# Kernel optimization log

Hardware: AMD Instinct MI355X
Metric: run time of the kernel (lower is better)

Reference implementation:

```python
import jax, jax.numpy as jnp
import numpy as np

NEG_SLOPE = 0.2


def gat_layer(x, src, dst, W, a_src, a_dst, b, n_nodes):
    # x: [N, F_in]; W: [F_in, H*C]; a_src/a_dst: [H, C]; b: [H*C]
    H, C = a_src.shape
    h = (x @ W).reshape(n_nodes, H, C)                    # [N, H, C]
    al_s = jnp.sum(h * a_src, axis=-1)                    # [N, H]
    al_d = jnp.sum(h * a_dst, axis=-1)                    # [N, H]
    e = jax.nn.leaky_relu(al_s[src] + al_d[dst], NEG_SLOPE)  # [E, H]
    # segment softmax over incoming edges of each dst node
    m = jax.ops.segment_max(e, dst, num_segments=n_nodes)   # [N, H]
    e = jnp.exp(e - m[dst])
    s = jax.ops.segment_sum(e, dst, num_segments=n_nodes)   # [N, H]
    alpha = e / (s[dst] + 1e-16)                             # [E, H]
    msg = h[src] * alpha[:, :, None]                         # [E, H, C]
    out = jax.ops.segment_sum(msg, dst, num_segments=n_nodes)
    return out.reshape(n_nodes, H * C) + b


def setup_inputs() -> dict:
    key = jax.random.key(0)
    ks = jax.random.split(key, 16)
    N, E = 50000, 800000
    F_in, Hd, heads, n_cls = 256, 256, 8, 64
    C = Hd // heads
    x = jax.random.normal(ks[0], (N, F_in), dtype=jnp.float32)
    edge_index = jax.random.randint(ks[1], (2, E), 0, N, dtype=jnp.int64)

    def lin(k, fin, fout):
        return jax.random.normal(k, (fin, fout), dtype=jnp.float32) / np.sqrt(fin).astype(np.float32)

    inp = {"x": x, "edge_index": edge_index}
    # layer 1: 256 -> 8 heads x 32
    inp["W1"] = lin(ks[2], F_in, Hd)
    inp["as1"] = jax.random.normal(ks[3], (heads, C), dtype=jnp.float32) * 0.1
    inp["ad1"] = jax.random.normal(ks[4], (heads, C), dtype=jnp.float32) * 0.1
    inp["b1"] = jnp.zeros((Hd,), dtype=jnp.float32)
    # layer 2: 256 -> 8 heads x 32
    inp["W2"] = lin(ks[5], Hd, Hd)
    inp["as2"] = jax.random.normal(ks[6], (heads, C), dtype=jnp.float32) * 0.1
    inp["ad2"] = jax.random.normal(ks[7], (heads, C), dtype=jnp.float32) * 0.1
    inp["b2"] = jnp.zeros((Hd,), dtype=jnp.float32)
    # layer 3: 256 -> 1 head x 64 (num_classes)
    inp["W3"] = lin(ks[8], Hd, n_cls)
    inp["as3"] = jax.random.normal(ks[9], (1, n_cls), dtype=jnp.float32) * 0.1
    inp["ad3"] = jax.random.normal(ks[10], (1, n_cls), dtype=jnp.float32) * 0.1
    inp["b3"] = jnp.zeros((n_cls,), dtype=jnp.float32)
    return inp


def reference(x, edge_index, W1, as1, ad1, b1, W2, as2, ad2, b2, W3, as3, ad3, b3):
    N = x.shape[0]
    # PyG GATConv default add_self_loops=True
    loop = jnp.arange(N, dtype=edge_index.dtype)
    src = jnp.concatenate([edge_index[0], loop])
    dst = jnp.concatenate([edge_index[1], loop])
    h = gat_layer(x, src, dst, W1, as1, ad1, b1, N)
    h = jax.nn.relu(h)  # dropout is identity at inference
    h = gat_layer(h, src, dst, W2, as2, ad2, b2, N)
    h = jax.nn.relu(h)
    out = gat_layer(h, src, dst, W3, as3, ad3, b3, N)
    return out
```

## Files before the change

### kernel.cpp

```cpp
#include <hip/hip_runtime.h>
#include <math.h>

#define NSLOPE 0.2f

typedef __attribute__((ext_vector_type(8))) short bf16x8;
typedef __attribute__((ext_vector_type(8))) unsigned short ushort8;
typedef __attribute__((ext_vector_type(4))) float f32x4;

static __device__ __forceinline__ float leaky(float e) {
    return e > 0.f ? e : NSLOPE * e;
}

static __device__ __forceinline__ float bfu(unsigned short u) {
    return __uint_as_float(((unsigned)u) << 16);
}

static __device__ __forceinline__ unsigned short f2bf_rne(float f) {
    unsigned b = __float_as_uint(f);
    unsigned r = b + 0x7fffu + ((b >> 16) & 1u);
    return (unsigned short)(r >> 16);
}

static __device__ __forceinline__ void split1(float f, unsigned short& hi,
                                              unsigned short& lo) {
    unsigned b = __float_as_uint(f);
    unsigned hb = b & 0xffff0000u;
    hi = (unsigned short)(hb >> 16);
    lo = (unsigned short)(__float_as_uint(f - __uint_as_float(hb)) >> 16);
}


__global__ void k_count(const int* __restrict__ dst, int* __restrict__ cnt, int E) {
    int i = blockIdx.x * blockDim.x + threadIdx.x;
    if (i < E) atomicAdd(&cnt[dst[i]], 1);
}

__global__ void k_scan_local(const int* __restrict__ cnt, int* __restrict__ ptr,
                             int* __restrict__ bsum, int N) {
    __shared__ int sd[256];
    int t = threadIdx.x;
    int i0 = blockIdx.x * 1024 + t * 4;
    int v0 = (i0 + 0 < N) ? cnt[i0 + 0] : 0;
    int v1 = (i0 + 1 < N) ? cnt[i0 + 1] : 0;
    int v2 = (i0 + 2 < N) ? cnt[i0 + 2] : 0;
    int v3 = (i0 + 3 < N) ? cnt[i0 + 3] : 0;
    int ts = v0 + v1 + v2 + v3;
    sd[t] = ts;
    __syncthreads();
    for (int o = 1; o < 256; o <<= 1) {
        int add = (t >= o) ? sd[t - o] : 0;
        __syncthreads();
        sd[t] += add;
        __syncthreads();
    }
    int run = sd[t] - ts;
    if (i0 + 0 < N) ptr[i0 + 0] = run; run += v0;
    if (i0 + 1 < N) ptr[i0 + 1] = run; run += v1;
    if (i0 + 2 < N) ptr[i0 + 2] = run; run += v2;
    if (i0 + 3 < N) ptr[i0 + 3] = run;
    if (t == 255) bsum[blockIdx.x] = sd[255];
}

__global__ void k_scan_add2(int* __restrict__ ptr, const int* __restrict__ bsum,
                            int N, int Et) {
    __shared__ int base;
    const int chunk = blockIdx.x >> 2;
    if (threadIdx.x == 0) {
        int s = 0;
        for (int b = 0; b < chunk; ++b) s += bsum[b];
        base = s;
    }
    __syncthreads();
    int i = blockIdx.x * 256 + threadIdx.x;
    if (i < N) ptr[i] += base;
    else if (i == N) ptr[N] = Et;
}

__global__ void k_copy(int* __restrict__ d, const int* __restrict__ s, int N) {
    int i = blockIdx.x * blockDim.x + threadIdx.x;
    if (i < N) d[i] = s[i];
}

__global__ void k_fillcsr(const int* __restrict__ ei, int* __restrict__ fptr,
                          int* __restrict__ srcs, int E, int Et) {
    int i = blockIdx.x * blockDim.x + threadIdx.x;
    if (i >= Et) return;
    int s, d;
    if (i < E) { s = ei[i]; d = ei[E + i]; }
    else       { s = d = i - E; }
    int pos = atomicAdd(&fptr[d], 1);
    srcs[pos] = s;
}

__global__ __launch_bounds__(256) void k_prep(
    int* __restrict__ cnt, int N,
    const float* __restrict__ x, unsigned short* __restrict__ xhi,
    unsigned short* __restrict__ xlo, int n8,
    const float* __restrict__ W1, unsigned short* __restrict__ w1h, unsigned short* __restrict__ w1l,
    const float* __restrict__ W2, unsigned short* __restrict__ w2h, unsigned short* __restrict__ w2l,
    const float* __restrict__ W3, unsigned short* __restrict__ w3h, unsigned short* __restrict__ w3l,
    int nset, int nsplit) {
    __shared__ float tile[32][33];
    const int b = blockIdx.x;
    const int tid = threadIdx.x;
    if (b < nset) {
        int i = b * 256 + tid;
        if (i < N) cnt[i] = 1;
    } else if (b < nset + nsplit) {
        int i = (b - nset) * 256 + tid;
        if (i < n8) {
            const float4 v0 = *reinterpret_cast<const float4*>(&x[(size_t)i * 8]);
            const float4 v1 = *reinterpret_cast<const float4*>(&x[(size_t)i * 8 + 4]);
            const float f[8] = {v0.x, v0.y, v0.z, v0.w, v1.x, v1.y, v1.z, v1.w};
            ushort8 h, l;
#pragma unroll
            for (int j = 0; j < 8; ++j) {
                unsigned short hj, lj;
                split1(f[j], hj, lj);
                h[j] = hj; l[j] = lj;
            }
            *reinterpret_cast<ushort8*>(&xhi[(size_t)i * 8]) = h;
            *reinterpret_cast<ushort8*>(&xlo[(size_t)i * 8]) = l;
        }
    } else {
        int tb = b - nset - nsplit;
        const float* B; unsigned short *H, *L;
        int M, bx, by;
        if (tb < 64)       { B = W1; H = w1h; L = w1l; M = 256; bx = (tb & 7) * 32; by = (tb >> 3) * 32; }
        else if (tb < 128) { tb -= 64;  B = W2; H = w2h; L = w2l; M = 256; bx = (tb & 7) * 32; by = (tb >> 3) * 32; }
        else               { tb -= 128; B = W3; H = w3h; L = w3l; M = 64;  bx = (tb & 1) * 32; by = (tb >> 1) * 32; }
        constexpr int K = 256;
        const int tx = tid & 31, ty = tid >> 5;
        for (int r = ty; r < 32; r += 8) tile[r][tx] = B[(size_t)(by + r) * M + bx + tx];
        __syncthreads();
        for (int r = ty; r < 32; r += 8) {
            unsigned short h, l;
            split1(tile[tx][r], h, l);
            H[(size_t)(bx + r) * K + by + tx] = h;
            L[(size_t)(bx + r) * K + by + tx] = l;
        }
    }
}


template <int HN, int CN>
__global__ __launch_bounds__(256) void k_gemm_s(const unsigned short* __restrict__ Ahi,
                                                const unsigned short* __restrict__ Alo,
                                                const unsigned short* __restrict__ Whi,
                                                const unsigned short* __restrict__ Wlo,
                                                const float* __restrict__ asrc,
                                                const float* __restrict__ adst,
                                                unsigned short* __restrict__ hb,
                                                float* __restrict__ als,
                                                float* __restrict__ ald,
                                                int N) {
    constexpr int K = 256;
    constexpr int M = HN * CN;
    __shared__ unsigned short Ah[64][40], Al[64][40], Bh[64][40], Bl[64][40];
    const int tid = threadIdx.x;
    const int lane = tid & 63;
    const int wid = tid >> 6;
    const int row0 = blockIdx.x * 64;
    const int col0 = blockIdx.y * 64;

    const int sr = tid >> 2;
    const int sk = (tid & 3) << 3;
    const int ga = row0 + sr;
    const size_t gaK = (size_t)ga * K;
    const size_t gcK = (size_t)(col0 + sr) * K;

    const int wr = (wid >> 1) * 32;
    const int wc = (wid & 1) * 32;
    const int fr = lane & 15;
    const int ko = (lane >> 4) * 8;

    f32x4 acc[2][2];
#pragma unroll
    for (int i = 0; i < 2; ++i)
#pragma unroll
        for (int j = 0; j < 2; ++j) acc[i][j] = (f32x4){0.f, 0.f, 0.f, 0.f};

    for (int k0 = 0; k0 < K; k0 += 32) {
        ushort8 ah = {0,0,0,0,0,0,0,0}, al = {0,0,0,0,0,0,0,0};
        if (ga < N) {
            ah = *reinterpret_cast<const ushort8*>(&Ahi[gaK + k0 + sk]);
            al = *reinterpret_cast<const ushort8*>(&Alo[gaK + k0 + sk]);
        }
        const ushort8 bh = *reinterpret_cast<const ushort8*>(&Whi[gcK + k0 + sk]);
        const ushort8 bl = *reinterpret_cast<const ushort8*>(&Wlo[gcK + k0 + sk]);
        *reinterpret_cast<ushort8*>(&Ah[sr][sk]) = ah;
        *reinterpret_cast<ushort8*>(&Al[sr][sk]) = al;
        *reinterpret_cast<ushort8*>(&Bh[sr][sk]) = bh;
        *reinterpret_cast<ushort8*>(&Bl[sr][sk]) = bl;
        __syncthreads();

        bf16x8 ahi[2], alo[2], bhi[2], blo[2];
#pragma unroll
        for (int i = 0; i < 2; ++i) {
            ahi[i] = *reinterpret_cast<const bf16x8*>(&Ah[wr + i * 16 + fr][ko]);
            alo[i] = *reinterpret_cast<const bf16x8*>(&Al[wr + i * 16 + fr][ko]);
        }
#pragma unroll
        for (int j = 0; j < 2; ++j) {
            bhi[j] = *reinterpret_cast<const bf16x8*>(&Bh[wc + j * 16 + fr][ko]);
            blo[j] = *reinterpret_cast<const bf16x8*>(&Bl[wc + j * 16 + fr][ko]);
        }
#pragma unroll
        for (int i = 0; i < 2; ++i)
#pragma unroll
            for (int j = 0; j < 2; ++j) {
                acc[i][j] = __builtin_amdgcn_mfma_f32_16x16x32_bf16(ahi[i], bhi[j], acc[i][j], 0, 0, 0);
                acc[i][j] = __builtin_amdgcn_mfma_f32_16x16x32_bf16(ahi[i], blo[j], acc[i][j], 0, 0, 0);
                acc[i][j] = __builtin_amdgcn_mfma_f32_16x16x32_bf16(alo[i], bhi[j], acc[i][j], 0, 0, 0);
            }
        __syncthreads();
    }

    const int orow = (lane >> 4) * 4;
    const int ocol = lane & 15;

#pragma unroll
    for (int i = 0; i < 2; ++i) {
#pragma unroll
        for (int r = 0; r < 4; ++r) {
            const int row = row0 + wr + i * 16 + orow + r;
            if (row < N) {
#pragma unroll
                for (int j = 0; j < 2; ++j) {
                    const int col = col0 + wc + j * 16 + ocol;
                    hb[(size_t)row * M + col] = f2bf_rne(acc[i][j][r]);
                }
            }
        }
    }

    const int c0 = col0 + wc;
    const float as0 = asrc[c0 + ocol],      as1 = asrc[c0 + 16 + ocol];
    const float ad0 = adst[c0 + ocol],      ad1 = adst[c0 + 16 + ocol];

    if constexpr (CN == 32) {
        const int head = c0 >> 5;
#pragma unroll
        for (int i = 0; i < 2; ++i) {
#pragma unroll
            for (int r = 0; r < 4; ++r) {
                float ps = acc[i][0][r] * as0 + acc[i][1][r] * as1;
                float pd = acc[i][0][r] * ad0 + acc[i][1][r] * ad1;
#pragma unroll
                for (int o = 1; o < 16; o <<= 1) {
                    ps += __shfl_xor(ps, o);
                    pd += __shfl_xor(pd, o);
                }
                const int row = row0 + wr + i * 16 + orow + r;
                if (ocol == 0 && row < N) {
                    als[(size_t)row * HN + head] = ps;
                    ald[(size_t)row * HN + head] = pd;
                }
            }
        }
    } else {
        __shared__ float part[2][64][2];
#pragma unroll
        for (int i = 0; i < 2; ++i) {
#pragma unroll
            for (int r = 0; r < 4; ++r) {
                float ps = acc[i][0][r] * as0 + acc[i][1][r] * as1;
                float pd = acc[i][0][r] * ad0 + acc[i][1][r] * ad1;
#pragma unroll
                for (int o = 1; o < 16; o <<= 1) {
                    ps += __shfl_xor(ps, o);
                    pd += __shfl_xor(pd, o);
                }
                if (ocol == 0) {
                    const int lr = wr + i * 16 + orow + r;
                    part[wc >> 5][lr][0] = ps;
                    part[wc >> 5][lr][1] = pd;
                }
            }
        }
        __syncthreads();
        if (tid < 64) {
            const int row = row0 + tid;
            if (row < N) {
                als[row] = part[0][tid][0] + part[1][tid][0];
                ald[row] = part[0][tid][1] + part[1][tid][1];
            }
        }
    }
}

template <int HN, int CN, int VEC, int P, bool OSPLIT>
__global__ __launch_bounds__(256) void k_agg6(const unsigned short* __restrict__ hb,
                                              const float* __restrict__ als,
                                              const float* __restrict__ ald,
                                              const int* __restrict__ ptr,
                                              const int* __restrict__ srcs,
                                              const float* __restrict__ bias,
                                              unsigned short* __restrict__ ohi,
                                              unsigned short* __restrict__ olo,
                                              float* __restrict__ out,
                                              int N, int relu) {
    constexpr int HC = HN * CN;
    constexpr int SUBS = 64 / HN;
    constexpr int GB = (SUBS < 16) ? SUBS : 16;
    const int l = threadIdx.x & 63;
    const int n = blockIdx.x * 4 + (threadIdx.x >> 6);
    if (n >= N) return;
    const int beg = ptr[n], end = ptr[n + 1];
    const int hd_e = l % HN;
    const int sub = l / HN;
    const float aldv = ald[(unsigned)n * HN + hd_e];

    float p[P];
    int   sr[P];
    float ssum = 0.f;
#pragma unroll
    for (int b = 0; b < P; ++b) {
        const int j = beg + b * SUBS + sub;
        float pv = 0.f; int s = 0;
        if (j < end) {
            s = srcs[j];
            pv = __expf(leaky(als[(unsigned)s * HN + hd_e] + aldv));
        }
        sr[b] = s; p[b] = pv; ssum += pv;
    }
    for (int j = beg + P * SUBS + sub; j < end; j += SUBS) {
        ssum += __expf(leaky(als[(unsigned)srcs[j] * HN + hd_e] + aldv));
    }
#pragma unroll
    for (int o = HN; o < 64; o <<= 1) ssum += __shfl_xor(ssum, o);
    const float inv = 1.f / (ssum + 1e-16f);

    const int ch = l * VEC;
    const int hl = ch / CN;
    float acc[VEC];
#pragma unroll
    for (int v = 0; v < VEC; ++v) acc[v] = 0.f;

#pragma unroll
    for (int b = 0; b < P; ++b) {
        const int j0 = beg + b * SUBS;
        if (j0 >= end) break;
        const float am = p[b] * inv;
#pragma unroll
        for (int cb = 0; cb < SUBS / GB; ++cb) {
            if (j0 + cb * GB >= end) break;
            float av[GB];
            if constexpr (VEC == 4) {
                ushort4 hv[GB];
#pragma unroll
                for (int c = 0; c < GB; ++c) {
                    const int ce = cb * GB + c;
                    const int s = __shfl(sr[b], ce * HN);
                    av[c] = __shfl(am, ce * HN + hl);
                    hv[c] = *reinterpret_cast<const ushort4*>(&hb[(unsigned)s * HC + ch]);
                }
#pragma unroll
                for (int c = 0; c < GB; ++c) {
                    acc[0] += av[c] * bfu(hv[c].x);
                    acc[1] += av[c] * bfu(hv[c].y);
                    acc[2] += av[c] * bfu(hv[c].z);
                    acc[3] += av[c] * bfu(hv[c].w);
                }
            } else {
                unsigned short hv[GB];
#pragma unroll
                for (int c = 0; c < GB; ++c) {
                    const int ce = cb * GB + c;
                    const int s = __shfl(sr[b], ce * HN);
                    av[c] = __shfl(am, ce * HN + hl);
                    hv[c] = hb[(unsigned)s * HC + ch];
                }
#pragma unroll
                for (int c = 0; c < GB; ++c) acc[0] += av[c] * bfu(hv[c]);
            }
        }
    }
    for (int j0 = beg + P * SUBS; j0 < end; j0 += SUBS) {
        const int j = j0 + sub;
        int sm = 0; float am = 0.f;
        if (j < end) {
            sm = srcs[j];
            am = __expf(leaky(als[(unsigned)sm * HN + hd_e] + aldv)) * inv;
        }
#pragma unroll
        for (int cb = 0; cb < SUBS / GB; ++cb) {
            if (j0 + cb * GB >= end) break;
            float av[GB];
            if constexpr (VEC == 4) {
                ushort4 hv[GB];
#pragma unroll
                for (int c = 0; c < GB; ++c) {
                    const int ce = cb * GB + c;
                    const int s = __shfl(sm, ce * HN);
                    av[c] = __shfl(am, ce * HN + hl);
                    hv[c] = *reinterpret_cast<const ushort4*>(&hb[(unsigned)s * HC + ch]);
                }
#pragma unroll
                for (int c = 0; c < GB; ++c) {
                    acc[0] += av[c] * bfu(hv[c].x);
                    acc[1] += av[c] * bfu(hv[c].y);
                    acc[2] += av[c] * bfu(hv[c].z);
                    acc[3] += av[c] * bfu(hv[c].w);
                }
            } else {
                unsigned short hv[GB];
#pragma unroll
                for (int c = 0; c < GB; ++c) {
                    const int ce = cb * GB + c;
                    const int s = __shfl(sm, ce * HN);
                    av[c] = __shfl(am, ce * HN + hl);
                    hv[c] = hb[(unsigned)s * HC + ch];
                }
#pragma unroll
                for (int c = 0; c < GB; ++c) acc[0] += av[c] * bfu(hv[c]);
            }
        }
    }

#pragma unroll
    for (int v = 0; v < VEC; ++v) {
        float o = acc[v] + bias[ch + v];
        if (relu) o = fmaxf(o, 0.f);
        acc[v] = o;
    }
    if constexpr (OSPLIT) {
        ushort4 ho, lo4;
        unsigned short h0, l0;
        split1(acc[0], h0, l0); ho.x = h0; lo4.x = l0;
        split1(acc[1], h0, l0); ho.y = h0; lo4.y = l0;
        split1(acc[2], h0, l0); ho.z = h0; lo4.z = l0;
        split1(acc[3], h0, l0); ho.w = h0; lo4.w = l0;
        *reinterpret_cast<ushort4*>(&ohi[(unsigned)n * HC + ch]) = ho;
        *reinterpret_cast<ushort4*>(&olo[(unsigned)n * HC + ch]) = lo4;
    } else if constexpr (VEC == 4) {
        float4 vout;
        vout.x = acc[0]; vout.y = acc[1]; vout.z = acc[2]; vout.w = acc[3];
        *reinterpret_cast<float4*>(&out[(unsigned)n * HC + ch]) = vout;
    } else {
        out[(unsigned)n * HC + ch] = acc[0];
    }
}


extern "C" void kernel_launch(void* const* d_in, const int* in_sizes, int n_in,
                              void* d_out, int out_size, void* d_ws, size_t ws_size,
                              hipStream_t stream) {
    const float* x   = (const float*)d_in[0];
    const int*   ei  = (const int*)d_in[1];
    const float* W1  = (const float*)d_in[2];
    const float* as1 = (const float*)d_in[3];
    const float* ad1 = (const float*)d_in[4];
    const float* b1  = (const float*)d_in[5];
    const float* W2  = (const float*)d_in[6];
    const float* as2 = (const float*)d_in[7];
    const float* ad2 = (const float*)d_in[8];
    const float* b2  = (const float*)d_in[9];
    const float* W3  = (const float*)d_in[10];
    const float* as3 = (const float*)d_in[11];
    const float* ad3 = (const float*)d_in[12];
    const float* b3  = (const float*)d_in[13];

    const int F  = 256;
    const int N  = in_sizes[0] / F;
    const int E  = in_sizes[1] / 2;
    const int Et = E + N;

    char* w = (char*)d_ws;
    auto alloc = [&](size_t bytes) {
        char* p = w;
        w += (bytes + 255) & ~(size_t)255;
        return p;
    };
    unsigned short* S0hi = (unsigned short*)alloc((size_t)N * F * 2);
    unsigned short* S0lo = (unsigned short*)alloc((size_t)N * F * 2);
    unsigned short* S1hi = (unsigned short*)alloc((size_t)N * F * 2);
    unsigned short* S1lo = (unsigned short*)alloc((size_t)N * F * 2);
    unsigned short* hB   = (unsigned short*)alloc((size_t)N * F * 2);
    unsigned short* Wt1hi = (unsigned short*)alloc((size_t)256 * 256 * 2);
    unsigned short* Wt1lo = (unsigned short*)alloc((size_t)256 * 256 * 2);
    unsigned short* Wt2hi = (unsigned short*)alloc((size_t)256 * 256 * 2);
    unsigned short* Wt2lo = (unsigned short*)alloc((size_t)256 * 256 * 2);
    unsigned short* Wt3hi = (unsigned short*)alloc((size_t)64 * 256 * 2);
    unsigned short* Wt3lo = (unsigned short*)alloc((size_t)64 * 256 * 2);
    float* als  = (float*)alloc((size_t)N * 8 * 4);
    float* ald  = (float*)alloc((size_t)N * 8 * 4);
    int*   cnt  = (int*)alloc((size_t)N * 4);
    int*   ptr  = (int*)alloc((size_t)(N + 1) * 4);
    int*   fptr = (int*)alloc((size_t)(N + 1) * 4);
    int*   srcs = (int*)alloc((size_t)Et * 4);
    int*   bsum = (int*)alloc(4096);

    const int n8 = N * F / 8;
    const int nset = (N + 255) / 256;
    const int nsplit = (n8 + 255) / 256;
    const int nprep = nset + nsplit + 64 + 64 + 16;

    hipLaunchKernelGGL(k_prep, dim3(nprep), dim3(256), 0, stream,
                       cnt, N, x, S0hi, S0lo, n8,
                       W1, Wt1hi, Wt1lo, W2, Wt2hi, Wt2lo, W3, Wt3hi, Wt3lo,
                       nset, nsplit);

    const int nb = (N + 1023) / 1024;
    hipLaunchKernelGGL(k_count,     dim3((E + 255) / 256),  dim3(256), 0, stream, ei + E, cnt, E);
    hipLaunchKernelGGL(k_scan_local,dim3(nb),               dim3(256), 0, stream, cnt, ptr, bsum, N);
    hipLaunchKernelGGL(k_scan_add2, dim3((N + 256) / 256),  dim3(256), 0, stream, ptr, bsum, N, Et);
    hipLaunchKernelGGL(k_copy,      dim3((N + 255) / 256),  dim3(256), 0, stream, fptr, ptr, N);
    hipLaunchKernelGGL(k_fillcsr,   dim3((Et + 255) / 256), dim3(256), 0, stream, ei, fptr, srcs, E, Et);

    const dim3 gN4((N + 3) / 4);
    const int gx = (N + 63) / 64;

    hipLaunchKernelGGL((k_gemm_s<8, 32>), dim3(gx, 4), dim3(256), 0, stream,
                       S0hi, S0lo, Wt1hi, Wt1lo, as1, ad1, hB, als, ald, N);
    hipLaunchKernelGGL((k_agg6<8, 32, 4, 8, true>), gN4, dim3(256), 0, stream,
                       hB, als, ald, ptr, srcs, b1, S1hi, S1lo, nullptr, N, 1);
    hipLaunchKernelGGL((k_gemm_s<8, 32>), dim3(gx, 4), dim3(256), 0, stream,
                       S1hi, S1lo, Wt2hi, Wt2lo, as2, ad2, hB, als, ald, N);
    hipLaunchKernelGGL((k_agg6<8, 32, 4, 8, true>), gN4, dim3(256), 0, stream,
                       hB, als, ald, ptr, srcs, b2, S0hi, S0lo, nullptr, N, 1);
    hipLaunchKernelGGL((k_gemm_s<1, 64>), dim3(gx, 1), dim3(256), 0, stream,
                       S0hi, S0lo, Wt3hi, Wt3lo, as3, ad3, hB, als, ald, N);
    hipLaunchKernelGGL((k_agg6<1, 64, 1, 2, false>), gN4, dim3(256), 0, stream,
                       hB, als, ald, ptr, srcs, b3, nullptr, nullptr, (float*)d_out, N, 0);
}
```

Measured before the change: 412.9 us.

## Add full-width 64x256 split-bf16 GEMM for the 256-column GAT layers

Adds a new GEMM kernel in which each block computes 64 rows by all 256 output columns, with each wave owning 64 columns (two heads), instead of a 2D grid of 64x64 tiles. The A tile (hi/lo bf16 split) is loaded once per block rather than four times, and the attention logits for both heads are reduced in registers. Layers 1 and 2 now use it, and the CN==32 path of the old kernel is removed, leaving only the LDS-partial path. In exchange, the block holds more accumulators and a larger weight tile in LDS, which may lower occupancy, and there are four times fewer blocks.

Result: faster. 403.9 us (-2.2%).

```diff
diff --git a/kernel.cpp b/kernel.cpp
--- a/kernel.cpp
+++ b/kernel.cpp
@@ -142,6 +142,129 @@
     }
 }
 
+__global__ __launch_bounds__(256) void k_gemm2(const unsigned short* __restrict__ Ahi,
+                                               const unsigned short* __restrict__ Alo,
+                                               const unsigned short* __restrict__ Whi,
+                                               const unsigned short* __restrict__ Wlo,
+                                               const float* __restrict__ asrc,
+                                               const float* __restrict__ adst,
+                                               unsigned short* __restrict__ hb,
+                                               float* __restrict__ als,
+                                               float* __restrict__ ald,
+                                               int N) {
+    constexpr int K = 256;
+    constexpr int M = 256;
+    __shared__ unsigned short Ah[64][36], Al[64][36];
+    __shared__ unsigned short Bh[256][36], Bl[256][36];
+    const int tid = threadIdx.x;
+    const int lane = tid & 63;
+    const int wid = tid >> 6;
+    const int row0 = blockIdx.x * 64;
+
+    const int sr = tid >> 2;
+    const int sk = (tid & 3) << 3;
+    const int ga = row0 + sr;
+    const size_t gaK = (size_t)ga * K;
+
+    const int wc0 = wid * 64;
+    const int fr = lane & 15;
+    const int ko = (lane >> 4) * 8;
+
+    f32x4 acc[4][4];
+#pragma unroll
+    for (int i = 0; i < 4; ++i)
+#pragma unroll
+        for (int j = 0; j < 4; ++j) acc[i][j] = (f32x4){0.f, 0.f, 0.f, 0.f};
+
+    for (int k0 = 0; k0 < K; k0 += 32) {
+        ushort8 ah = {0,0,0,0,0,0,0,0}, al = {0,0,0,0,0,0,0,0};
+        if (ga < N) {
+            ah = *reinterpret_cast<const ushort8*>(&Ahi[gaK + k0 + sk]);
+            al = *reinterpret_cast<const ushort8*>(&Alo[gaK + k0 + sk]);
+        }
+        *reinterpret_cast<ushort8*>(&Ah[sr][sk]) = ah;
+        *reinterpret_cast<ushort8*>(&Al[sr][sk]) = al;
+#pragma unroll
+        for (int p = 0; p < 4; ++p) {
+            const int m = sr + 64 * p;
+            const size_t gm = (size_t)m * K + k0 + sk;
+            *reinterpret_cast<ushort8*>(&Bh[m][sk]) =
+                *reinterpret_cast<const ushort8*>(&Whi[gm]);
+            *reinterpret_cast<ushort8*>(&Bl[m][sk]) =
+                *reinterpret_cast<const ushort8*>(&Wlo[gm]);
+        }
+        __syncthreads();
+
+        bf16x8 ahi[4], alo4[4];
+#pragma unroll
+        for (int i = 0; i < 4; ++i) {
+            ahi[i]  = *reinterpret_cast<const bf16x8*>(&Ah[i * 16 + fr][ko]);
+            alo4[i] = *reinterpret_cast<const bf16x8*>(&Al[i * 16 + fr][ko]);
+        }
+#pragma unroll
+        for (int j = 0; j < 4; ++j) {
+            const bf16x8 bh = *reinterpret_cast<const bf16x8*>(&Bh[wc0 + j * 16 + fr][ko]);
+            const bf16x8 bl = *reinterpret_cast<const bf16x8*>(&Bl[wc0 + j * 16 + fr][ko]);
+#pragma unroll
+            for (int i = 0; i < 4; ++i) {
+                acc[i][j] = __builtin_amdgcn_mfma_f32_16x16x32_bf16(ahi[i], bh, acc[i][j], 0, 0, 0);
+                acc[i][j] = __builtin_amdgcn_mfma_f32_16x16x32_bf16(ahi[i], bl, acc[i][j], 0, 0, 0);
+                acc[i][j] = __builtin_amdgcn_mfma_f32_16x16x32_bf16(alo4[i], bh, acc[i][j], 0, 0, 0);
+            }
+        }
+        __syncthreads();
+    }
+
+    const int orow = (lane >> 4) * 4;
+    const int ocol = lane & 15;
+
+#pragma unroll
+    for (int i = 0; i < 4; ++i) {
+#pragma unroll
+        for (int r = 0; r < 4; ++r) {
+            const int row = row0 + i * 16 + orow + r;
+            if (row < N) {
+#pragma unroll
+                for (int j = 0; j < 4; ++j) {
+                    const int col = wc0 + j * 16 + ocol;
+                    hb[(size_t)row * M + col] = f2bf_rne(acc[i][j][r]);
+                }
+            }
+        }
+    }
+
+    const float as0 = asrc[wc0 + ocol],      as1 = asrc[wc0 + 16 + ocol];
+    const float as2 = asrc[wc0 + 32 + ocol], as3 = asrc[wc0 + 48 + ocol];
+    const float ad0 = adst[wc0 + ocol],      ad1 = adst[wc0 + 16 + ocol];
+    const float ad2 = adst[wc0 + 32 + ocol], ad3 = adst[wc0 + 48 + ocol];
+    const int headA = wc0 >> 5, headB = headA + 1;
+
+#pragma unroll
+    for (int i = 0; i < 4; ++i) {
+#pragma unroll
+        for (int r = 0; r < 4; ++r) {
+            float psA = acc[i][0][r] * as0 + acc[i][1][r] * as1;
+            float pdA = acc[i][0][r] * ad0 + acc[i][1][r] * ad1;
+            float psB = acc[i][2][r] * as2 + acc[i][3][r] * as3;
+            float pdB = acc[i][2][r] * ad2 + acc[i][3][r] * ad3;
+#pragma unroll
+            for (int o = 1; o < 16; o <<= 1) {
+                psA += __shfl_xor(psA, o);
+                pdA += __shfl_xor(pdA, o);
+                psB += __shfl_xor(psB, o);
+                pdB += __shfl_xor(pdB, o);
+            }
+            const int row = row0 + i * 16 + orow + r;
+            if (ocol == 0 && row < N) {
+                als[(size_t)row * 8 + headA] = psA;
+                ald[(size_t)row * 8 + headA] = pdA;
+                als[(size_t)row * 8 + headB] = psB;
+                ald[(size_t)row * 8 + headB] = pdB;
+            }
+        }
+    }
+}
+
 
 template <int HN, int CN>
 __global__ __launch_bounds__(256) void k_gemm_s(const unsigned short* __restrict__ Ahi,
@@ -238,27 +361,7 @@
     const float as0 = asrc[c0 + ocol],      as1 = asrc[c0 + 16 + ocol];
     const float ad0 = adst[c0 + ocol],      ad1 = adst[c0 + 16 + ocol];
 
-    if constexpr (CN == 32) {
-        const int head = c0 >> 5;
-#pragma unroll
-        for (int i = 0; i < 2; ++i) {
-#pragma unroll
-            for (int r = 0; r < 4; ++r) {
-                float ps = acc[i][0][r] * as0 + acc[i][1][r] * as1;
-                float pd = acc[i][0][r] * ad0 + acc[i][1][r] * ad1;
-#pragma unroll
-                for (int o = 1; o < 16; o <<= 1) {
-                    ps += __shfl_xor(ps, o);
-                    pd += __shfl_xor(pd, o);
-                }
-                const int row = row0 + wr + i * 16 + orow + r;
-                if (ocol == 0 && row < N) {
-                    als[(size_t)row * HN + head] = ps;
-                    ald[(size_t)row * HN + head] = pd;
-                }
-            }
-        }
-    } else {
+    {
         __shared__ float part[2][64][2];
 #pragma unroll
         for (int i = 0; i < 2; ++i) {
@@ -511,11 +614,11 @@
     const dim3 gN4((N + 3) / 4);
     const int gx = (N + 63) / 64;
 
-    hipLaunchKernelGGL((k_gemm_s<8, 32>), dim3(gx, 4), dim3(256), 0, stream,
+    hipLaunchKernelGGL(k_gemm2, dim3(gx), dim3(256), 0, stream,
                        S0hi, S0lo, Wt1hi, Wt1lo, as1, ad1, hB, als, ald, N);
     hipLaunchKernelGGL((k_agg6<8, 32, 4, 8, true>), gN4, dim3(256), 0, stream,
                        hB, als, ald, ptr, srcs, b1, S1hi, S1lo, nullptr, N, 1);
-    hipLaunchKernelGGL((k_gemm_s<8, 32>), dim3(gx, 4), dim3(256), 0, stream,
+    hipLaunchKernelGGL(k_gemm2, dim3(gx), dim3(256), 0, stream,
                        S1hi, S1lo, Wt2hi, Wt2lo, as2, ad2, hB, als, ald, N);
     hipLaunchKernelGGL((k_agg6<8, 32, 4, 8, true>), gN4, dim3(256), 0, stream,
                        hB, als, ald, ptr, srcs, b2, S0hi, S0lo, nullptr, N, 1);
```
